# Optimization experiments

Hardware: AMD Instinct MI355X
Metric: run time of the kernel (lower is better)

The kernel has to match this reference:

```python
import jax, jax.numpy as jnp
import numpy as np

B, H, S, D = 4, 16, 4096, 64

def _phi(x):
    # feature map for linear attention: elu(x) + 1 (positive features)
    return jax.nn.elu(x) + 1.0

def setup_inputs() -> dict:
    key = jax.random.key(0)
    kq, kk, kv = jax.random.split(key, 3)
    return {
        "query": jax.random.normal(kq, (B, H, S, D), dtype=jnp.float32),
        "key": jax.random.normal(kk, (B, H, S, D), dtype=jnp.float32),
        "value": jax.random.normal(kv, (B, H, S, D), dtype=jnp.float32),
        "attention_mask": jnp.ones((B, S), dtype=jnp.float32),
    }

def reference(query, key, value, attention_mask):
    head_dim = query.shape[-1]
    scale = 1.0 / jnp.sqrt(jnp.sqrt(jnp.float32(head_dim)))
    q = query * scale
    k = key * scale
    phi_q = _phi(q)
    phi_k = _phi(k)
    m = attention_mask[:, None, :, None]  # [B,1,S,1]
    phi_q = phi_q * m
    phi_k = phi_k * m
    # kv_term: [B,H,D,Dv]
    kv_term = jnp.einsum("bhsd,bhse->bhde", phi_k, value)
    out = jnp.einsum("bhsd,bhde->bhse", phi_q, kv_term)
    # normalizer: phi_q @ sum_s phi_k -> [B,H,S,1]
    k_one = jnp.sum(phi_k, axis=-2)  # [B,H,D]
    normalizer = jnp.einsum("bhsd,bhd->bhs", phi_q, k_one)[..., None]
    return out / (normalizer + 1e-8)
```

## Files before the change

### kernel.cpp

```cpp
#include <hip/hip_runtime.h>

#define BDIM 4
#define HDIM 16
#define SDIM 4096
#define DDIM 64
#define NBH (BDIM * HDIM)

#define NC 16
#define BH_STRIDE (DDIM * DDIM + DDIM)
#define CHUNK_FLOATS (NBH * BH_STRIDE)

__device__ __forceinline__ float phi_f(float x) {
    return x > 0.0f ? x + 1.0f : __expf(x);
}

template<bool ATOMIC>
__global__ __launch_bounds__(256, 2) void la_phase1(
    const float* __restrict__ K, const float* __restrict__ V,
    const float* __restrict__ mask, float* __restrict__ outp, int chunk_rows)
{
    __shared__ __align__(16) float smem[8320];

    const int bh = blockIdx.y;
    const int b  = bh / HDIM;
    const int t  = threadIdx.x;
    const int w  = t >> 6;
    const int l  = t & 63;
    const int rowq = l >> 4;
    const int c4   = (l & 15) << 2;
    const int d0   = (l >> 3) << 3;
    const int e0   = (l & 7) << 3;

    float* kT = smem + w * 1024;

    const float* Kb = K + (size_t)bh * SDIM * DDIM;
    const float* Vb = V + (size_t)bh * SDIM * DDIM;
    const float* mb = mask + (size_t)b * SDIM;
    const float scale = 0.35355339059327373f;

    const int rows_per_wave = chunk_rows >> 2;
    const int s_wave = blockIdx.x * chunk_rows + w * rows_per_wave;
    const int ntiles = rows_per_wave >> 4;

    float acc[8][8] = {};
    float k1s[4] = {0.f, 0.f, 0.f, 0.f};

    float4 kr[4]; float mmr[4];
    #pragma unroll
    for (int j = 0; j < 4; ++j) {
        const int s = s_wave + rowq + (j << 2);
        kr[j]  = *(const float4*)(Kb + (size_t)s * DDIM + c4);
        mmr[j] = mb[s];
    }

    for (int tt = 0; tt < ntiles; ++tt) {
        #pragma unroll
        for (int j = 0; j < 4; ++j) {
            float4 p;
            p.x = phi_f(kr[j].x * scale) * mmr[j];
            p.y = phi_f(kr[j].y * scale) * mmr[j];
            p.z = phi_f(kr[j].z * scale) * mmr[j];
            p.w = phi_f(kr[j].w * scale) * mmr[j];
            k1s[0] += p.x; k1s[1] += p.y; k1s[2] += p.z; k1s[3] += p.w;
            *(float4*)&kT[(rowq + (j << 2)) * DDIM + c4] = p;
        }
        if (tt + 1 < ntiles) {
            #pragma unroll
            for (int j = 0; j < 4; ++j) {
                const int s = s_wave + ((tt + 1) << 4) + rowq + (j << 2);
                kr[j]  = *(const float4*)(Kb + (size_t)s * DDIM + c4);
                mmr[j] = mb[s];
            }
        }

        const int s_tile = s_wave + (tt << 4);
        #pragma unroll
        for (int ss = 0; ss < 16; ++ss) {
            const float4 a0 = *(const float4*)&kT[ss * DDIM + d0];
            const float4 a1 = *(const float4*)&kT[ss * DDIM + d0 + 4];
            const float4 v0 = *(const float4*)(Vb + (size_t)(s_tile + ss) * DDIM + e0);
            const float4 v1 = *(const float4*)(Vb + (size_t)(s_tile + ss) * DDIM + e0 + 4);
            const float av[8] = {a0.x, a0.y, a0.z, a0.w, a1.x, a1.y, a1.z, a1.w};
            const float vv[8] = {v0.x, v0.y, v0.z, v0.w, v1.x, v1.y, v1.z, v1.w};
            #pragma unroll
            for (int i = 0; i < 8; ++i)
                #pragma unroll
                for (int j = 0; j < 8; ++j)
                    acc[i][j] += av[i] * vv[j];
        }
    }

    #pragma unroll
    for (int i = 0; i < 4; ++i) {
        k1s[i] += __shfl_xor(k1s[i], 16);
        k1s[i] += __shfl_xor(k1s[i], 32);
    }

    __syncthreads();
    float* bufA = smem;
    float* bufB = smem + 4160;
    if (w < 2) {
        float* Bp = w ? bufB : bufA;
        #pragma unroll
        for (int i = 0; i < 8; ++i) {
            *(float4*)&Bp[(d0 + i) * DDIM + e0]     = make_float4(acc[i][0], acc[i][1], acc[i][2], acc[i][3]);
            *(float4*)&Bp[(d0 + i) * DDIM + e0 + 4] = make_float4(acc[i][4], acc[i][5], acc[i][6], acc[i][7]);
        }
        if (l < 16) *(float4*)&Bp[4096 + (l << 2)] = make_float4(k1s[0], k1s[1], k1s[2], k1s[3]);
    }
    __syncthreads();
    if (w >= 2) {
        float* Bp = (w == 3) ? bufB : bufA;
        #pragma unroll
        for (int i = 0; i < 8; ++i) {
            float4 x0 = *(float4*)&Bp[(d0 + i) * DDIM + e0];
            float4 x1 = *(float4*)&Bp[(d0 + i) * DDIM + e0 + 4];
            x0.x += acc[i][0]; x0.y += acc[i][1]; x0.z += acc[i][2]; x0.w += acc[i][3];
            x1.x += acc[i][4]; x1.y += acc[i][5]; x1.z += acc[i][6]; x1.w += acc[i][7];
            *(float4*)&Bp[(d0 + i) * DDIM + e0]     = x0;
            *(float4*)&Bp[(d0 + i) * DDIM + e0 + 4] = x1;
        }
        if (l < 16) {
            float4 x = *(float4*)&Bp[4096 + (l << 2)];
            x.x += k1s[0]; x.y += k1s[1]; x.z += k1s[2]; x.w += k1s[3];
            *(float4*)&Bp[4096 + (l << 2)] = x;
        }
    }
    __syncthreads();

    float* base = ATOMIC ? (outp + (size_t)bh * BH_STRIDE)
                         : (outp + ((size_t)blockIdx.x * NBH + bh) * BH_STRIDE);
    for (int g = t; g < BH_STRIDE / 4; g += 256) {
        const float4 xa = ((const float4*)bufA)[g];
        const float4 xb = ((const float4*)bufB)[g];
        if (ATOMIC) {
            atomicAdd(&base[4 * g + 0], xa.x + xb.x);
            atomicAdd(&base[4 * g + 1], xa.y + xb.y);
            atomicAdd(&base[4 * g + 2], xa.z + xb.z);
            atomicAdd(&base[4 * g + 3], xa.w + xb.w);
        } else {
            *(float4*)&base[4 * g] = make_float4(xa.x + xb.x, xa.y + xb.y, xa.z + xb.z, xa.w + xb.w);
        }
    }
}

__global__ __launch_bounds__(256) void la_reduce(
    const float* __restrict__ part, float* __restrict__ fin)
{
    const int g = blockIdx.x * 256 + threadIdx.x;
    const float4* p4 = (const float4*)part;
    float4 s = p4[g];
    #pragma unroll
    for (int c = 1; c < NC; ++c) {
        const float4 v = p4[(size_t)c * (CHUNK_FLOATS / 4) + g];
        s.x += v.x; s.y += v.y; s.z += v.z; s.w += v.w;
    }
    ((float4*)fin)[g] = s;
}

__global__ __launch_bounds__(256, 2) void la_phase2(
    const float* __restrict__ Q, const float* __restrict__ mask,
    const float* __restrict__ fin_all, float* __restrict__ out)
{
    __shared__ __align__(16) float kvL[DDIM * DDIM];
    __shared__ __align__(16) float koL[DDIM];

    const int bh = blockIdx.y;
    const int b  = bh / HDIM;
    const int t  = threadIdx.x;
    const int w  = t >> 6;
    const int l  = t & 63;
    const int e0 = (l & 7) << 3;
    const int r0 = blockIdx.x * 256 + (w << 6) + ((l >> 3) << 3);

    const float* fin = fin_all + (size_t)bh * BH_STRIDE;
    {
        const float4* src = (const float4*)fin;
        float4* dst = (float4*)kvL;
        #pragma unroll
        for (int k = 0; k < 4; ++k) dst[t + 256 * k] = src[t + 256 * k];
        if (t < DDIM) koL[t] = fin[DDIM * DDIM + t];
    }
    __syncthreads();

    const float* Qb = Q + (size_t)bh * SDIM * DDIM;
    const float* mb = mask + (size_t)b * SDIM;
    const float scale = 0.35355339059327373f;

    float acc[8][8] = {};
    float nrm[8] = {0.f, 0.f, 0.f, 0.f, 0.f, 0.f, 0.f, 0.f};

    #pragma unroll 1
    for (int dt = 0; dt < 16; ++dt) {
        const int d4 = dt << 2;
        float4 qp[8];
        #pragma unroll
        for (int i = 0; i < 8; ++i) {
            const float4 q = *(const float4*)(Qb + (size_t)(r0 + i) * DDIM + d4);
            qp[i].x = phi_f(q.x * scale);
            qp[i].y = phi_f(q.y * scale);
            qp[i].z = phi_f(q.z * scale);
            qp[i].w = phi_f(q.w * scale);
        }
        const float4 ko4 = *(const float4*)&koL[d4];
        #pragma unroll
        for (int dd = 0; dd < 4; ++dd) {
            const float4 b0 = *(const float4*)&kvL[(d4 + dd) * DDIM + e0];
            const float4 b1 = *(const float4*)&kvL[(d4 + dd) * DDIM + e0 + 4];
            const float bv[8] = {b0.x, b0.y, b0.z, b0.w, b1.x, b1.y, b1.z, b1.w};
            const float kod = (dd == 0) ? ko4.x : (dd == 1) ? ko4.y : (dd == 2) ? ko4.z : ko4.w;
            #pragma unroll
            for (int i = 0; i < 8; ++i) {
                const float a = (dd == 0) ? qp[i].x : (dd == 1) ? qp[i].y : (dd == 2) ? qp[i].z : qp[i].w;
                nrm[i] += a * kod;
                #pragma unroll
                for (int j = 0; j < 8; ++j)
                    acc[i][j] += a * bv[j];
            }
        }
    }

    float* ob = out + (size_t)bh * SDIM * DDIM;
    #pragma unroll
    for (int i = 0; i < 8; ++i) {
        const float mm  = mb[r0 + i];
        const float inv = mm / (mm * nrm[i] + 1e-8f);
        *(float4*)(ob + (size_t)(r0 + i) * DDIM + e0) =
            make_float4(acc[i][0] * inv, acc[i][1] * inv, acc[i][2] * inv, acc[i][3] * inv);
        *(float4*)(ob + (size_t)(r0 + i) * DDIM + e0 + 4) =
            make_float4(acc[i][4] * inv, acc[i][5] * inv, acc[i][6] * inv, acc[i][7] * inv);
    }
}

extern "C" void kernel_launch(void* const* d_in, const int* in_sizes, int n_in,
                              void* d_out, int out_size, void* d_ws, size_t ws_size,
                              hipStream_t stream) {
    const float* Q = (const float*)d_in[0];
    const float* K = (const float*)d_in[1];
    const float* V = (const float*)d_in[2];
    const float* M = (const float*)d_in[3];
    float* out = (float*)d_out;

    const size_t chunk_bytes = (size_t)CHUNK_FLOATS * sizeof(float);

    if (ws_size >= (size_t)(NC + 1) * chunk_bytes) {
        float* part = (float*)d_ws;
        float* fin  = part + (size_t)NC * CHUNK_FLOATS;
        la_phase1<false><<<dim3(NC, NBH), dim3(256), 0, stream>>>(K, V, M, part, SDIM / NC);
        la_reduce<<<dim3(CHUNK_FLOATS / 4 / 256), dim3(256), 0, stream>>>(part, fin);
        la_phase2<<<dim3(SDIM / 256, NBH), dim3(256), 0, stream>>>(Q, M, fin, out);
    } else {
        float* fin = (float*)d_ws;
        hipMemsetAsync(d_ws, 0, chunk_bytes, stream);
        la_phase1<true><<<dim3(NC, NBH), dim3(256), 0, stream>>>(K, V, M, fin, SDIM / NC);
        la_phase2<<<dim3(SDIM / 256, NBH), dim3(256), 0, stream>>>(Q, M, fin, out);
    }
}
```

Baseline: 286.5 us.

## Stage phi(Q) through LDS with coalesced double-buffered loads in phase2

Phase2 now has each lane load one Q row slice coalesced, apply phi once, and write it to a double-buffered LDS tile. The tile is then read back as 4 rows per thread, with the next d-slice prefetched while the current one is used. Rows per thread drop from 8 to 4 and rows per block from 256 to 128, which doubles the grid, and launch bounds rise to 4 blocks per CU. The aim is to remove redundant uncoalesced Q loads and repeated phi evaluation across the 8 lanes sharing a row, and to raise occupancy. In exchange it adds LDS traffic, and each kv value read from LDS now feeds fewer FMAs.

Result: faster. 254.5 us (-11.2%).

```diff
diff --git a/kernel.cpp b/kernel.cpp
--- a/kernel.cpp
+++ b/kernel.cpp
@@ -144,6 +144,7 @@
     }
 }
 
+template<int NCT>
 __global__ __launch_bounds__(256) void la_reduce(
     const float* __restrict__ part, float* __restrict__ fin)
 {
@@ -151,83 +152,103 @@
     const float4* p4 = (const float4*)part;
     float4 s = p4[g];
     #pragma unroll
-    for (int c = 1; c < NC; ++c) {
+    for (int c = 1; c < NCT; ++c) {
         const float4 v = p4[(size_t)c * (CHUNK_FLOATS / 4) + g];
         s.x += v.x; s.y += v.y; s.z += v.z; s.w += v.w;
     }
     ((float4*)fin)[g] = s;
 }
 
-__global__ __launch_bounds__(256, 2) void la_phase2(
+__global__ __launch_bounds__(256, 4) void la_phase2(
     const float* __restrict__ Q, const float* __restrict__ mask,
     const float* __restrict__ fin_all, float* __restrict__ out)
 {
     __shared__ __align__(16) float kvL[DDIM * DDIM];
     __shared__ __align__(16) float koL[DDIM];
+    __shared__ __align__(16) float pqw[4][2][32][4];
 
     const int bh = blockIdx.y;
     const int b  = bh / HDIM;
     const int t  = threadIdx.x;
     const int w  = t >> 6;
     const int l  = t & 63;
+    const int g  = l >> 3;
     const int e0 = (l & 7) << 3;
-    const int r0 = blockIdx.x * 256 + (w << 6) + ((l >> 3) << 3);
+    const int rbase = blockIdx.x * 128 + (w << 5);
+    const int rown  = l & 31;
 
     const float* fin = fin_all + (size_t)bh * BH_STRIDE;
     {
         const float4* src = (const float4*)fin;
         float4* dst = (float4*)kvL;
         #pragma unroll
-        for (int k = 0; k < 4; ++k) dst[t + 256 * k] = src[t + 256 * k];
+        for (int k2 = 0; k2 < 4; ++k2) dst[t + 256 * k2] = src[t + 256 * k2];
         if (t < DDIM) koL[t] = fin[DDIM * DDIM + t];
     }
-    __syncthreads();
-
-    const float* Qb = Q + (size_t)bh * SDIM * DDIM;
-    const float* mb = mask + (size_t)b * SDIM;
+
+    const float* Qb   = Q + (size_t)bh * SDIM * DDIM;
+    const float* mb   = mask + (size_t)b * SDIM;
+    const float* Qrow = Qb + (size_t)(rbase + rown) * DDIM;
     const float scale = 0.35355339059327373f;
 
-    float acc[8][8] = {};
-    float nrm[8] = {0.f, 0.f, 0.f, 0.f, 0.f, 0.f, 0.f, 0.f};
+    float4 q0 = *(const float4*)(Qrow);
+    float4 qn = *(const float4*)(Qrow + 4);
+    __syncthreads();
+
+    {
+        float4 p;
+        p.x = phi_f(q0.x * scale);
+        p.y = phi_f(q0.y * scale);
+        p.z = phi_f(q0.z * scale);
+        p.w = phi_f(q0.w * scale);
+        if (l < 32) *(float4*)&pqw[w][0][rown][0] = p;
+    }
+
+    float acc[4][8] = {};
+    float nrm[4] = {0.f, 0.f, 0.f, 0.f};
 
     #pragma unroll 1
     for (int dt = 0; dt < 16; ++dt) {
-        const int d4 = dt << 2;
-        float4 qp[8];
-        #pragma unroll
-        for (int i = 0; i < 8; ++i) {
-            const float4 q = *(const float4*)(Qb + (size_t)(r0 + i) * DDIM + d4);
-            qp[i].x = phi_f(q.x * scale);
-            qp[i].y = phi_f(q.y * scale);
-            qp[i].z = phi_f(q.z * scale);
-            qp[i].w = phi_f(q.w * scale);
-        }
+        const int d4  = dt << 2;
+        const int cur = dt & 1;
+        if (dt < 15) {
+            float4 p;
+            p.x = phi_f(qn.x * scale);
+            p.y = phi_f(qn.y * scale);
+            p.z = phi_f(qn.z * scale);
+            p.w = phi_f(qn.w * scale);
+            if (l < 32) *(float4*)&pqw[w][cur ^ 1][rown][0] = p;
+            if (dt < 14) qn = *(const float4*)(Qrow + ((dt + 2) << 2));
+        }
+        float4 ar[4];
+        #pragma unroll
+        for (int i = 0; i < 4; ++i)
+            ar[i] = *(const float4*)&pqw[w][cur][(g << 2) + i][0];
         const float4 ko4 = *(const float4*)&koL[d4];
         #pragma unroll
         for (int dd = 0; dd < 4; ++dd) {
             const float4 b0 = *(const float4*)&kvL[(d4 + dd) * DDIM + e0];
             const float4 b1 = *(const float4*)&kvL[(d4 + dd) * DDIM + e0 + 4];
-            const float bv[8] = {b0.x, b0.y, b0.z, b0.w, b1.x, b1.y, b1.z, b1.w};
             const float kod = (dd == 0) ? ko4.x : (dd == 1) ? ko4.y : (dd == 2) ? ko4.z : ko4.w;
             #pragma unroll
-            for (int i = 0; i < 8; ++i) {
-                const float a = (dd == 0) ? qp[i].x : (dd == 1) ? qp[i].y : (dd == 2) ? qp[i].z : qp[i].w;
+            for (int i = 0; i < 4; ++i) {
+                const float a = (dd == 0) ? ar[i].x : (dd == 1) ? ar[i].y : (dd == 2) ? ar[i].z : ar[i].w;
                 nrm[i] += a * kod;
-                #pragma unroll
-                for (int j = 0; j < 8; ++j)
-                    acc[i][j] += a * bv[j];
+                acc[i][0] += a * b0.x; acc[i][1] += a * b0.y; acc[i][2] += a * b0.z; acc[i][3] += a * b0.w;
+                acc[i][4] += a * b1.x; acc[i][5] += a * b1.y; acc[i][6] += a * b1.z; acc[i][7] += a * b1.w;
             }
         }
     }
 
     float* ob = out + (size_t)bh * SDIM * DDIM;
     #pragma unroll
-    for (int i = 0; i < 8; ++i) {
-        const float mm  = mb[r0 + i];
+    for (int i = 0; i < 4; ++i) {
+        const int r  = rbase + (g << 2) + i;
+        const float mm  = mb[r];
         const float inv = mm / (mm * nrm[i] + 1e-8f);
-        *(float4*)(ob + (size_t)(r0 + i) * DDIM + e0) =
+        *(float4*)(ob + (size_t)r * DDIM + e0) =
             make_float4(acc[i][0] * inv, acc[i][1] * inv, acc[i][2] * inv, acc[i][3] * inv);
-        *(float4*)(ob + (size_t)(r0 + i) * DDIM + e0 + 4) =
+        *(float4*)(ob + (size_t)r * DDIM + e0 + 4) =
             make_float4(acc[i][4] * inv, acc[i][5] * inv, acc[i][6] * inv, acc[i][7] * inv);
     }
 }
@@ -247,12 +268,12 @@
         float* part = (float*)d_ws;
         float* fin  = part + (size_t)NC * CHUNK_FLOATS;
         la_phase1<false><<<dim3(NC, NBH), dim3(256), 0, stream>>>(K, V, M, part, SDIM / NC);
-        la_reduce<<<dim3(CHUNK_FLOATS / 4 / 256), dim3(256), 0, stream>>>(part, fin);
-        la_phase2<<<dim3(SDIM / 256, NBH), dim3(256), 0, stream>>>(Q, M, fin, out);
+        la_reduce<NC><<<dim3(CHUNK_FLOATS / 4 / 256), dim3(256), 0, stream>>>(part, fin);
+        la_phase2<<<dim3(SDIM / 128, NBH), dim3(256), 0, stream>>>(Q, M, fin, out);
     } else {
         float* fin = (float*)d_ws;
         hipMemsetAsync(d_ws, 0, chunk_bytes, stream);
         la_phase1<true><<<dim3(NC, NBH), dim3(256), 0, stream>>>(K, V, M, fin, SDIM / NC);
-        la_phase2<<<dim3(SDIM / 256, NBH), dim3(256), 0, stream>>>(Q, M, fin, out);
-    }
-}
+        la_phase2<<<dim3(SDIM / 128, NBH), dim3(256), 0, stream>>>(Q, M, fin, out);
+    }
+}
```
